# Kernel tuning notes

Measured on AMD Instinct MI355X. Metric: run time of the kernel, lower is better.

Reference implementation:

```python
import jax, jax.numpy as jnp
import numpy as np

ANCHORS = np.array([[4.63,1.97,1.74],[6.93,2.51,2.84],[6.37,2.85,3.19],[10.5,2.94,3.47],
                    [12.29,2.9,3.87],[0.5,2.53,0.98],[2.11,0.77,1.47],[1.7,0.6,1.28],
                    [0.73,0.67,1.77],[0.41,0.41,1.07]], dtype=np.float32)  # [10,3] nuScenes anchor sizes
BINS = 20          # anchor_size_bins
TEXT_DIM = 3 * BINS
NUM_PROPOSALS = 200
NMS_K = 3


def _vector_values():
    la = np.log(ANCHORS)
    return np.linspace(la.min() - 0.1, la.max() - 0.1, BINS).astype(np.float32)


def _anchor_vecs_normed():
    # soft_relu_bin_vectors: soft-bin log-anchors into BINS bins per dim, dim-major flatten
    vals = _vector_values()
    inc = vals[1] - vals[0]
    la = np.log(ANCHORS)                                      # [10,3]
    v = np.clip((la[:, :, None] - vals[None, None, :]) / inc, 0.0, 1.0)  # [10,3,BINS]
    v = v.reshape(10, TEXT_DIM)
    return (v / (1e-8 + np.linalg.norm(v, axis=1, keepdims=True))).astype(np.float32)


def conv2d(x, w, b=None):
    y = jax.lax.conv_general_dilated(x, w, (1, 1), 'SAME',
                                     dimension_numbers=('NCHW', 'OIHW', 'NCHW'))
    if b is not None:
        y = y + b[None, :, None, None]
    return y


def iou_sim_vec(a):
    # vectorized form of the triple-nested loop: prod over dims of min/max ratio
    mn = jnp.minimum(a[:, None, :], a[None, :, :])
    mx = jnp.maximum(a[:, None, :], a[None, :, :])
    return jnp.prod(mn / mx, axis=-1)                         # [10,10]


def setup_inputs() -> dict:
    key = jax.random.key(0)
    ks = jax.random.split(key, 8)
    B, Cin, hid, H, W = 2, 512, 128, 180, 180
    feats = jax.random.normal(ks[0], (B, Cin, H, W), jnp.float32)
    w_shared = jax.random.normal(ks[1], (hid, Cin, 3, 3), jnp.float32) * 0.02
    b_shared = jnp.zeros((hid,), jnp.float32)
    w_bb = jax.random.normal(ks[2], (hid, hid, 3, 3), jnp.float32) * 0.05
    gamma_bb = jnp.ones((hid,), jnp.float32)
    beta_bb = jnp.zeros((hid,), jnp.float32)
    w_hm = jax.random.normal(ks[3], (TEXT_DIM, hid, 3, 3), jnp.float32) * 0.05
    b_hm = jnp.zeros((TEXT_DIM,), jnp.float32)
    thr_scale = jnp.ones((1,), jnp.float32)                   # Threshold2d scale
    logit_scale = jnp.ones((1,), jnp.float32) * np.log(1.0 / 0.07)
    logit_bias = jnp.ones((1,), jnp.float32) * (-10.0)
    w_enc = jax.random.normal(ks[4], (hid, 3), jnp.float32) * 0.1  # Conv1d(3->hid, k=1)
    anchor_vecs = jnp.asarray(_anchor_vecs_normed())
    xs = jnp.arange(W, dtype=jnp.float32) + 0.5
    ys = jnp.arange(H, dtype=jnp.float32) + 0.5
    gy, gx = jnp.meshgrid(ys, xs, indexing='ij')
    bev_pos = jnp.stack([gx.reshape(-1), gy.reshape(-1)], axis=-1)  # [H*W, 2]
    return dict(feats=feats, w_shared=w_shared, b_shared=b_shared, w_bb=w_bb,
                gamma_bb=gamma_bb, beta_bb=beta_bb, w_hm=w_hm, b_hm=b_hm,
                thr_scale=thr_scale, logit_scale=logit_scale, logit_bias=logit_bias,
                w_enc=w_enc, anchor_vecs=anchor_vecs, bev_pos=bev_pos)


def reference(feats, w_shared, b_shared, w_bb, gamma_bb, beta_bb, w_hm, b_hm,
              thr_scale, logit_scale, logit_bias, w_enc, anchor_vecs, bev_pos):
    B, _, H, W = feats.shape
    # shared conv
    lidar_feat = conv2d(feats, w_shared, b_shared)            # [B,hid,H,W]
    # BasicBlock2D: conv + (inference) BN + ReLU
    x = conv2d(lidar_feat, w_bb)
    x = jax.nn.relu(x * gamma_bb[None, :, None, None] + beta_bb[None, :, None, None])
    # heatmap conv -> Threshold2d (sigmoid((x - thresholds) * scale))
    vec = conv2d(x, w_hm, b_hm)                               # [B,60,H,W]
    thresholds = jnp.asarray(np.tile(_vector_values(), 3))[None, :, None, None]
    vec = jax.nn.sigmoid((vec - thresholds) * thr_scale[0])
    # cosine sim vs normalized anchor bin-vectors -> per-class heatmap
    vecn = vec / (1e-8 + jnp.linalg.norm(vec, axis=1, keepdims=True))
    sim = jnp.einsum('bchw,kc->bkhw', vecn, anchor_vecs)      # [B,10,H,W]
    heatmap = jax.nn.sigmoid(logit_scale[0] * sim + logit_bias[0])
    # NMS: keep only local maxima within nms_kernel_size window
    local_max = jax.lax.reduce_window(heatmap, -jnp.inf, jax.lax.max,
                                      (1, 1, NMS_K, NMS_K), (1, 1, 1, 1), 'SAME')
    hm_nms = jnp.where(heatmap == local_max, heatmap, 0.0)
    # top-k proposals over classes x positions
    flat = hm_nms.reshape(B, -1)                              # [B, 10*H*W]
    top_scores, top_idx = jax.lax.top_k(flat, NUM_PROPOSALS)
    top_labels = top_idx // (H * W)                           # [B,P]
    top_pos = top_idx % (H * W)                               # [B,P]
    # gather proposal features, heatmap scores and bev positions
    hid = lidar_feat.shape[1]
    lidar_flat = lidar_feat.reshape(B, hid, H * W)
    idx_f = jnp.broadcast_to(top_pos[:, None, :], (B, hid, NUM_PROPOSALS))
    query_feat = jnp.take_along_axis(lidar_flat, idx_f, axis=2)  # [B,hid,P]
    hm_flat = heatmap.reshape(B, 10, H * W)
    idx_h = jnp.broadcast_to(top_pos[:, None, :], (B, 10, NUM_PROPOSALS))
    query_hm_score = jnp.take_along_axis(hm_flat, idx_h, axis=2)  # [B,10,P]
    query_pos = bev_pos[top_pos]                              # [B,P,2]
    # anchor value encoding (Conv1d(3->hid,k=1) on log-anchor sizes of top classes)
    top_anchor = jnp.log(jnp.asarray(ANCHORS))[top_labels]    # [B,P,3]
    query_feat = query_feat + jnp.einsum('cd,bpd->bcp', w_enc, top_anchor)
    sims = iou_sim_vec(jnp.asarray(ANCHORS))                  # [10,10] anchor IoU similarity
    return heatmap, top_scores, top_labels, query_feat, query_pos, query_hm_score, sims
```

## Files before the change

### kernel.cpp

```cpp
#include <hip/hip_runtime.h>
#include <math.h>


#define HW 180
#define NPIX 32400
#define NCLS 10
#define NPROP 200
#define HID 128
#define TDIM 60
#define NBIG (NCLS*NPIX)

#define TH_LO  (-0.9915981193)
#define TH_STEP (0.1789675812)

__constant__ float c_anchors[10][3] = {
  {4.63f,1.97f,1.74f},{6.93f,2.51f,2.84f},{6.37f,2.85f,3.19f},{10.5f,2.94f,3.47f},
  {12.29f,2.9f,3.87f},{0.5f,2.53f,0.98f},{2.11f,0.77f,1.47f},{1.7f,0.6f,1.28f},
  {0.73f,0.67f,1.77f},{0.41f,0.41f,1.07f}};

using f16x8 = _Float16 __attribute__((ext_vector_type(8)));
using f16x4 = _Float16 __attribute__((ext_vector_type(4)));
using f32x4 = float    __attribute__((ext_vector_type(4)));

#define GLD_LDS16(g, l) __builtin_amdgcn_global_load_lds( \
    (__attribute__((address_space(1))) void*)(g), \
    (__attribute__((address_space(3))) void*)(l), 16, 0, 0)

template<int CIN, int KS, int HALVES>
__global__ void transpose_w_mfma(const float* __restrict__ w, _Float16* __restrict__ dst,
                                 int cout) {
  const int N = HALVES * KS * 36864;
  int i = blockIdx.x * 256 + threadIdx.x;
  if (i >= N) return;
  int j = i & 7;
  int lane = (i >> 3) & 63;
  int mf = (i >> 9) & 3;
  int rest = i >> 11;
  int t = rest % 9; rest /= 9;
  int plane = rest & 1; rest >>= 1;
  int ks = rest % KS; int h = rest / KS;
  int co = h * 64 + mf * 16 + (lane & 15);
  int ch = ks * 32 + (lane >> 4) * 8 + j;
  float v = (co < cout) ? w[((size_t)co * CIN + ch) * 9 + t] : 0.f;
  _Float16 hi = (_Float16)v;
  dst[i] = plane ? (_Float16)(v - (float)hi) : hi;
}

__global__ __launch_bounds__(256)
void convert_feats(const float* __restrict__ feats, _Float16* __restrict__ X1) {
  int px = blockIdx.x * 256 + threadIdx.x;
  int b = blockIdx.y >> 4, ks = blockIdx.y & 15;
  if (px >= NPIX) return;
  const float* src = feats + ((size_t)(b * 512 + ks * 32)) * NPIX + px;
  float v[32];
#pragma unroll
  for (int c = 0; c < 32; ++c) v[c] = src[(size_t)c * NPIX];
  f16x8 hv[4], lv[4];
#pragma unroll
  for (int c = 0; c < 32; ++c) {
    _Float16 h = (_Float16)v[c];
    hv[c >> 3][c & 7] = h;
    lv[c >> 3][c & 7] = (_Float16)(v[c] - (float)h);
  }
  size_t ob = ((size_t)(b * 16 + ks) * NPIX + px) * 32;
#pragma unroll
  for (int i = 0; i < 4; ++i) {
    *(f16x8*)(X1 + ob + i * 8) = hv[i];
    *(f16x8*)(X1 + 33177600u + ob + i * 8) = lv[i];
  }
}

template<int KS, int EPI>
__global__ __launch_bounds__(256, 2)
void conv_mfma(const _Float16* __restrict__ X, const _Float16* __restrict__ W,
               const float* __restrict__ p0, const float* __restrict__ p1,
               float* __restrict__ out0, _Float16* __restrict__ outX,
               const float* __restrict__ thr_scale, const float* __restrict__ logit_scale,
               const float* __restrict__ logit_bias, const float* __restrict__ anchor_vecs) {
  constexpr unsigned XPS = 2u * KS * NPIX * 32;
  extern __shared__ _Float16 dlds[];
  _Float16* lds_x = dlds;
  _Float16* lds_w = dlds + 20736;
  float* lds_av = (float*)(dlds + 39168);

  const int x0 = blockIdx.x * 16;
  const int y0 = blockIdx.y * 16;
  const int b  = (EPI == 2) ? blockIdx.z : (blockIdx.z >> 1);
  const int h  = (EPI == 2) ? 0 : (blockIdx.z & 1);
  const int tid = threadIdx.x;
  const int wave = tid >> 6;
  const int lane = tid & 63;
  const int xl = lane & 15, kg = lane >> 4;

  {
    unsigned* p = (unsigned*)lds_x;
    for (int i = tid; i < 10368; i += 256) p[i] = 0u;
    if (EPI == 2)
      for (int i = tid; i < 600; i += 256) lds_av[i] = anchor_vecs[i];
  }

  unsigned offs[11]; unsigned okb = 0;
#pragma unroll
  for (int s = 0; s < 11; ++s) {
    int inst = wave + 4 * s;
    int c = inst * 64 + lane;
    bool valid = (inst < 41) && (c < 2592);
    int plane = (c >= 1296) ? 1 : 0;
    int cc = c - plane * 1296;
    int px = cc >> 2, q = cc & 3;
    int r = px / 18, xx = px - r * 18;
    int gy = y0 - 1 + r, gx = x0 - 1 + xx;
    bool ok = valid && ((unsigned)gy < 180u) && ((unsigned)gx < 180u);
    offs[s] = ok ? ((unsigned)((b * KS) * NPIX + gy * 180 + gx) * 32u + (unsigned)q * 8u
                    + (unsigned)plane * XPS) : 0u;
    okb |= (ok ? 1u : 0u) << s;
  }

  f32x4 acc[4][4];
#pragma unroll
  for (int mf = 0; mf < 4; ++mf)
#pragma unroll
    for (int f = 0; f < 4; ++f) acc[mf][f] = (f32x4){0.f, 0.f, 0.f, 0.f};

  const _Float16* gwb = W + (size_t)(h * KS) * 36864;
  for (int ks = 0; ks < KS; ++ks) {
    __syncthreads();
    const unsigned kof = (unsigned)ks * (NPIX * 32u);
#pragma unroll
    for (int s = 0; s < 11; ++s) {
      if (okb & (1u << s))
        GLD_LDS16(X + (size_t)(offs[s] + kof), lds_x + (wave + 4 * s) * 512);
    }
    const _Float16* gw = gwb + (size_t)ks * 36864;
#pragma unroll
    for (int s = 0; s < 9; ++s) {
      int c2 = wave + 4 * s;
      GLD_LDS16(gw + c2 * 512 + lane * 8, lds_w + c2 * 512);
    }
    __syncthreads();

#pragma unroll
    for (int t = 0; t < 9; ++t) {
      const int ky = t / 3, kx = t % 3;
      f16x8 bh[4], bl[4];
#pragma unroll
      for (int f = 0; f < 4; ++f) {
        int R = 4 * wave + f;
        int lo = ((R + ky) * 18 + xl + kx) * 32 + kg * 8;
        bh[f] = *(const f16x8*)(lds_x + lo);
        bl[f] = *(const f16x8*)(lds_x + 10368 + lo);
      }
      const _Float16* wt = lds_w + t * 2048 + lane * 8;
      f16x8 ah[4];
#pragma unroll
      for (int mf = 0; mf < 4; ++mf) ah[mf] = *(const f16x8*)(wt + mf * 512);
#pragma unroll
      for (int mf = 0; mf < 4; ++mf)
#pragma unroll
        for (int f = 0; f < 4; ++f) {
          acc[mf][f] = __builtin_amdgcn_mfma_f32_16x16x32_f16(ah[mf], bh[f], acc[mf][f], 0, 0, 0);
          acc[mf][f] = __builtin_amdgcn_mfma_f32_16x16x32_f16(ah[mf], bl[f], acc[mf][f], 0, 0, 0);
        }
    }
    __syncthreads();
#pragma unroll
    for (int s = 0; s < 9; ++s) {
      int c2 = wave + 4 * s;
      GLD_LDS16(gw + 18432 + c2 * 512 + lane * 8, lds_w + c2 * 512);
    }
    __syncthreads();

#pragma unroll
    for (int t = 0; t < 9; ++t) {
      const int ky = t / 3, kx = t % 3;
      f16x8 bh[4];
#pragma unroll
      for (int f = 0; f < 4; ++f) {
        int R = 4 * wave + f;
        int lo = ((R + ky) * 18 + xl + kx) * 32 + kg * 8;
        bh[f] = *(const f16x8*)(lds_x + lo);
      }
      const _Float16* wt = lds_w + t * 2048 + lane * 8;
      f16x8 al[4];
#pragma unroll
      for (int mf = 0; mf < 4; ++mf) al[mf] = *(const f16x8*)(wt + mf * 512);
#pragma unroll
      for (int mf = 0; mf < 4; ++mf)
#pragma unroll
        for (int f = 0; f < 4; ++f)
          acc[mf][f] = __builtin_amdgcn_mfma_f32_16x16x32_f16(al[mf], bh[f], acc[mf][f], 0, 0, 0);
    }
  }

  const int x = x0 + xl;
  if (EPI != 2) {
    if (x >= HW) return;
#pragma unroll
    for (int mf = 0; mf < 4; ++mf) {
      const int cobase = h * 64 + mf * 16 + kg * 4;
      f32x4 q0 = *(const f32x4*)(p0 + cobase);
      f32x4 q1 = (EPI == 1) ? *(const f32x4*)(p1 + cobase) : (f32x4){0.f,0.f,0.f,0.f};
#pragma unroll
      for (int f = 0; f < 4; ++f) {
        const int y = y0 + 4 * wave + f;
        if (y >= HW) continue;
        const int kso = cobase >> 5, c32 = cobase & 31;
        size_t nidx = ((size_t)(b * 4 + kso) * NPIX + (size_t)y * 180 + x) * 32 + c32;
        if (EPI == 0) {
          f32x4 v;
          f16x4 h4, l4;
#pragma unroll
          for (int r = 0; r < 4; ++r) {
            float z = acc[mf][f][r] + q0[r];
            v[r] = z;
            _Float16 hh = (_Float16)z;
            h4[r] = hh;
            l4[r] = (_Float16)(z - (float)hh);
          }
          *(f32x4*)(out0 + nidx) = v;
          *(f16x4*)(outX + nidx) = h4;
          *(f16x4*)(outX + 8294400u + nidx) = l4;
        } else {
          f16x4 h4, l4;
#pragma unroll
          for (int r = 0; r < 4; ++r) {
            float z = fmaf(acc[mf][f][r], q0[r], q1[r]);
            z = fmaxf(z, 0.f);
            _Float16 hh = (_Float16)z;
            h4[r] = hh;
            l4[r] = (_Float16)(z - (float)hh);
          }
          *(f16x4*)(outX + nidx) = h4;
          *(f16x4*)(outX + 8294400u + nidx) = l4;
        }
      }
    }
  } else {
    const float s  = thr_scale[0];
    const float ls = logit_scale[0];
    const float lb = logit_bias[0];
    float bh4[4][4], th4[4][4];
    bool vmask[4];
#pragma unroll
    for (int mf = 0; mf < 4; ++mf) {
      const int cb = mf * 16 + kg * 4;
      vmask[mf] = (cb < TDIM);
#pragma unroll
      for (int r = 0; r < 4; ++r) {
        bh4[mf][r] = vmask[mf] ? p0[cb + r] : 0.f;
        th4[mf][r] = (float)(TH_LO + (double)((cb + r) % 20) * TH_STEP);
      }
    }
#pragma unroll
    for (int f = 0; f < 4; ++f) {
      const int y = y0 + 4 * wave + f;
      float v[4][4];
      float s2 = 0.f;
#pragma unroll
      for (int mf = 0; mf < 4; ++mf)
#pragma unroll
        for (int r = 0; r < 4; ++r) {
          float z = acc[mf][f][r] + bh4[mf][r];
          float t = (z - th4[mf][r]) * s;
          float vv = vmask[mf] ? 1.f / (1.f + expf(-t)) : 0.f;
          v[mf][r] = vv;
          s2 = fmaf(vv, vv, s2);
        }
      s2 += __shfl_xor(s2, 16);
      s2 += __shfl_xor(s2, 32);
      const float rs = 1.f / (1e-8f + sqrtf(s2));
      float hm[10];
#pragma unroll
      for (int k = 0; k < 10; ++k) {
        float d = 0.f;
#pragma unroll
        for (int mf = 0; mf < 4; ++mf) {
          if (true) {
            const int cb = mf * 16 + kg * 4;
            f32x4 a = vmask[mf] ? *(const f32x4*)(lds_av + k * TDIM + cb)
                                : (f32x4){0.f, 0.f, 0.f, 0.f};
#pragma unroll
            for (int r = 0; r < 4; ++r) d = fmaf(v[mf][r], a[r], d);
          }
        }
        d += __shfl_xor(d, 16);
        d += __shfl_xor(d, 32);
        hm[k] = 1.f / (1.f + expf(-fmaf(ls, d * rs, lb)));
      }
      if (y < HW && x < HW) {
#pragma unroll
        for (int j = 0; j < 3; ++j) {
          int k = kg + 4 * j;
          if (k < NCLS)
            out0[((size_t)(b * NCLS + k) * HW + y) * HW + x] = hm[k];
        }
      }
    }
  }
}

__global__ void sims_kernel(float* __restrict__ out_sims) {
  int t = threadIdx.x;
  if (t < 100) {
    int i = t / 10, j = t % 10;
    float r = 1.f;
#pragma unroll
    for (int d = 0; d < 3; ++d) {
      float ai = c_anchors[i][d], aj = c_anchors[j][d];
      r *= fminf(ai, aj) / fmaxf(ai, aj);
    }
    out_sims[t] = r;
  }
}

__global__ __launch_bounds__(256)
void nms_kernel(const float* __restrict__ hm, float* __restrict__ ckey,
                int* __restrict__ cidx, int* __restrict__ cnt) {
  __shared__ int lcnt[2];
  __shared__ int lbase[2];
  const int tid = threadIdx.x;
  if (tid < 2) lcnt[tid] = 0;
  __syncthreads();

  int i = blockIdx.x * 256 + tid;
  bool surv = false; float v = 0.f; int bk = 0, p = 0;
  if (i < 2 * NBIG) {
    int x = i % HW; int y = (i / HW) % HW; int plane = i / NPIX;
    v = hm[i];
    float m = v;
#pragma unroll
    for (int dy = -1; dy <= 1; ++dy)
#pragma unroll
      for (int dx = -1; dx <= 1; ++dx) {
        int yy = y + dy, xx = x + dx;
        if ((unsigned)yy < (unsigned)HW && (unsigned)xx < (unsigned)HW)
          m = fmaxf(m, hm[((size_t)plane * NPIX) + yy * HW + xx]);
      }
    if (v == m) {
      surv = true;
      bk = i / NBIG;
      p = atomicAdd(&lcnt[bk], 1);
    }
  }
  __syncthreads();
  if (tid < 2 && lcnt[tid] > 0)
    lbase[tid] = atomicAdd(&cnt[tid], lcnt[tid]);
  __syncthreads();
  if (surv) {
    int slot = lbase[bk] + p;
    ckey[(size_t)bk * NBIG + slot] = v;
    cidx[(size_t)bk * NBIG + slot] = i - bk * NBIG;
  }
}

__global__ __launch_bounds__(1024)
void topk_kernel(const float* __restrict__ ckey, const int* __restrict__ cidx,
                 const int* __restrict__ cnt, const float* __restrict__ heatmap,
                 const float* __restrict__ bev_pos, float* __restrict__ out,
                 int* __restrict__ iws) {
  const int b = blockIdx.x;
  const int tid = threadIdx.x;
  const float* keys = ckey + (size_t)b * NBIG;
  const int* idxs = cidx + (size_t)b * NBIG;

  __shared__ unsigned hist[256];
  __shared__ unsigned sh_prefix;
  __shared__ int sh_want, sh_n;
  __shared__ int cntGT, cntTie;
  __shared__ unsigned gt_key[256], gt_idx[256];
  __shared__ unsigned tie_idx[2048];

  if (tid == 0) sh_n = cnt[b];
  __syncthreads();
  const int n = sh_n;

  unsigned prefix = 0; int want = NPROP;
  for (int shift = 24; shift >= 0; shift -= 8) {
    if (tid < 256) hist[tid] = 0u;
    __syncthreads();
    for (int i = tid; i < n; i += 1024) {
      unsigned k = __float_as_uint(keys[i]);
      bool match = (shift == 24) || ((k >> (shift + 8)) == (prefix >> (shift + 8)));
      if (match) atomicAdd(&hist[(k >> shift) & 255], 1u);
    }
    __syncthreads();
    if (tid == 0) {
      int cum = 0; int bsel = 0; sh_want = want;
      for (int bin = 255; bin >= 0; --bin) {
        cum += (int)hist[bin];
        if (cum >= want) { bsel = bin; sh_want = want - (cum - (int)hist[bin]); break; }
      }
      sh_prefix = prefix | ((unsigned)bsel << shift);
      cntGT = 0; cntTie = 0;
    }
    __syncthreads();
    prefix = sh_prefix; want = sh_want;
    __syncthreads();
  }
  const unsigned T = prefix;

  for (int i = tid; i < n; i += 1024) {
    unsigned k = __float_as_uint(keys[i]);
    if (k > T) {
      int p = atomicAdd(&cntGT, 1);
      if (p < 256) { gt_key[p] = k; gt_idx[p] = (unsigned)idxs[i]; }
    } else if (k == T) {
      int p = atomicAdd(&cntTie, 1);
      if (p < 2048) tie_idx[p] = (unsigned)idxs[i];
    }
  }
  __syncthreads();
  const int nGT = min(cntGT, 256);
  const int nTie = min(cntTie, 2048);

  for (int i = tid; i < 256; i += 1024)
    if (i >= nGT) { gt_key[i] = 0u; gt_idx[i] = 0xFFFFFFFFu; }
  for (int i = tid; i < 2048; i += 1024)
    if (i >= nTie) tie_idx[i] = 0xFFFFFFFFu;
  __syncthreads();

  for (int k2 = 2; k2 <= 256; k2 <<= 1) {
    for (int j = k2 >> 1; j > 0; j >>= 1) {
      for (int i = tid; i < 256; i += 1024) {
        int ixj = i ^ j;
        if (ixj > i) {
          unsigned ka = gt_key[i], kb = gt_key[ixj];
          unsigned ia = gt_idx[i], ib = gt_idx[ixj];
          bool firstA = (ka > kb) || (ka == kb && ia < ib);
          bool up = ((i & k2) == 0);
          if (up ? !firstA : firstA) {
            gt_key[i] = kb; gt_key[ixj] = ka;
            gt_idx[i] = ib; gt_idx[ixj] = ia;
          }
        }
      }
      __syncthreads();
    }
  }
  for (int k2 = 2; k2 <= 2048; k2 <<= 1) {
    for (int j = k2 >> 1; j > 0; j >>= 1) {
      for (int i = tid; i < 2048; i += 1024) {
        int ixj = i ^ j;
        if (ixj > i) {
          unsigned ia = tie_idx[i], ib = tie_idx[ixj];
          bool firstA = ia < ib;
          bool up = ((i & k2) == 0);
          if (up ? !firstA : firstA) { tie_idx[i] = ib; tie_idx[ixj] = ia; }
        }
      }
      __syncthreads();
    }
  }

  for (int r = tid; r < NPROP; r += 1024) {
    unsigned idx; float score;
    if (r < nGT) { idx = gt_idx[r]; score = __uint_as_float(gt_key[r]); }
    else         { idx = tie_idx[r - nGT]; score = __uint_as_float(T); }
    int label = (int)(idx / NPIX);
    int pos = (int)(idx - (unsigned)label * NPIX);
    out[648000 + b * NPROP + r] = score;
    out[648400 + b * NPROP + r] = (float)label;
    out[700000 + (b * NPROP + r) * 2 + 0] = bev_pos[pos * 2 + 0];
    out[700000 + (b * NPROP + r) * 2 + 1] = bev_pos[pos * 2 + 1];
#pragma unroll
    for (int k = 0; k < NCLS; ++k)
      out[700800 + (b * NCLS + k) * NPROP + r] = heatmap[(size_t)(b * NCLS + k) * NPIX + pos];
    iws[b * NPROP + r] = pos;
    iws[2 * NPROP + b * NPROP + r] = label;
  }
}

__global__ void gather_qf_kernel(const float* __restrict__ lidar, const float* __restrict__ w_enc,
                                 const int* __restrict__ iws, float* __restrict__ out_qf) {
  int p = blockIdx.x % NPROP;
  int b = blockIdx.x / NPROP;
  int c = threadIdx.x;
  int pos = iws[b * NPROP + p];
  int label = iws[2 * NPROP + b * NPROP + p];
  float la0 = logf(c_anchors[label][0]);
  float la1 = logf(c_anchors[label][1]);
  float la2 = logf(c_anchors[label][2]);
  float dot = w_enc[c * 3 + 0] * la0 + w_enc[c * 3 + 1] * la1 + w_enc[c * 3 + 2] * la2;
  float g = lidar[((size_t)(b * 4 + (c >> 5)) * NPIX + pos) * 32 + (c & 31)];
  out_qf[((size_t)b * HID + c) * NPROP + p] = g + dot;
}

extern "C" void kernel_launch(void* const* d_in, const int* in_sizes, int n_in,
                              void* d_out, int out_size, void* d_ws, size_t ws_size,
                              hipStream_t stream) {
  (void)in_sizes; (void)n_in; (void)out_size; (void)ws_size;
  const float* feats       = (const float*)d_in[0];
  const float* w_shared    = (const float*)d_in[1];
  const float* b_shared    = (const float*)d_in[2];
  const float* w_bb        = (const float*)d_in[3];
  const float* gamma_bb    = (const float*)d_in[4];
  const float* beta_bb     = (const float*)d_in[5];
  const float* w_hm        = (const float*)d_in[6];
  const float* b_hm        = (const float*)d_in[7];
  const float* thr_scale   = (const float*)d_in[8];
  const float* logit_scale = (const float*)d_in[9];
  const float* logit_bias  = (const float*)d_in[10];
  const float* w_enc       = (const float*)d_in[11];
  const float* anchor_vecs = (const float*)d_in[12];
  const float* bev_pos     = (const float*)d_in[13];
  float* out = (float*)d_out;

  float* ws = (float*)d_ws;
  size_t off = 0;
  _Float16* X1 = (_Float16*)(ws + off); off += 33177600;
  _Float16* X2 = (_Float16*)(ws + off); off += 8294400;
  float* lidarN = ws + off; off += 8294400;
  _Float16* X3 = (_Float16*)(ws + off); off += 8294400;
  _Float16* W1 = (_Float16*)(ws + off); off += 589824;
  _Float16* W2 = (_Float16*)(ws + off); off += 147456;
  _Float16* W3 = (_Float16*)(ws + off); off += 73728;
  float* ckey  = ws + off; off += (size_t)2 * NBIG;
  int*   cidx  = (int*)(ws + off); off += (size_t)2 * NBIG;
  int*   iws   = (int*)(ws + off); off += 800;
  int*   cnt   = (int*)(ws + off);

  transpose_w_mfma<512,16,2><<<(2*16*36864 + 255)/256, 256, 0, stream>>>(w_shared, W1, 128);
  transpose_w_mfma<128, 4,2><<<(2*4*36864  + 255)/256, 256, 0, stream>>>(w_bb, W2, 128);
  transpose_w_mfma<128, 4,1><<<(1*4*36864  + 255)/256, 256, 0, stream>>>(w_hm, W3, 60);
  convert_feats<<<dim3(127, 32), 256, 0, stream>>>(feats, X1);

  const unsigned CONV_LDS = (20736 + 18432) * sizeof(_Float16);
  const unsigned HEAD_LDS = CONV_LDS + 600 * sizeof(float);
  dim3 cgrid(12, 12, 4);
  conv_mfma<16,0><<<cgrid, 256, CONV_LDS, stream>>>(X1, W1, b_shared, nullptr, lidarN, X2,
                                                    nullptr, nullptr, nullptr, nullptr);
  conv_mfma<4, 1><<<cgrid, 256, CONV_LDS, stream>>>(X2, W2, gamma_bb, beta_bb, nullptr, X3,
                                                    nullptr, nullptr, nullptr, nullptr);
  dim3 hgrid(12, 12, 2);
  conv_mfma<4, 2><<<hgrid, 256, HEAD_LDS, stream>>>(X3, W3, b_hm, nullptr, out, nullptr,
                                                    thr_scale, logit_scale, logit_bias,
                                                    anchor_vecs);

  sims_kernel<<<1, 128, 0, stream>>>(out + 704800);
  hipMemsetAsync(cnt, 0, 2 * sizeof(int), stream);
  nms_kernel<<<(2*NBIG + 255)/256, 256, 0, stream>>>(out, ckey, cidx, cnt);
  topk_kernel<<<2, 1024, 0, stream>>>(ckey, cidx, cnt, out, bev_pos, out, iws);
  gather_qf_kernel<<<2*NPROP, 128, 0, stream>>>(lidarN, w_enc, iws, out + 648800);
}
```

Before: 586.3 us.

## Restructure conv MFMA loop by kernel column to reuse input fragments across rows

Permutes the weight layout so taps are grouped by kernel column (kx), then splits each channel slice into three phases of 3 taps. Each phase loads hi and lo weight planes together, and the six input row fragments are read from LDS once and reused across the three ky taps. The hi and lo weight passes are also merged into one loop. This cuts redundant LDS reads of input fragments and the LDS weight footprint, in exchange for more barriers per K-slice (3 syncs instead of 2 weight loads) and more live registers.

```diff
diff --git a/kernel.cpp b/kernel.cpp
--- a/kernel.cpp
+++ b/kernel.cpp
@@ -36,7 +36,8 @@
   int lane = (i >> 3) & 63;
   int mf = (i >> 9) & 3;
   int rest = i >> 11;
-  int t = rest % 9; rest /= 9;
+  int tsl = rest % 9; rest /= 9;
+  int t = (tsl % 3) * 3 + (tsl / 3);
   int plane = rest & 1; rest >>= 1;
   int ks = rest % KS; int h = rest / KS;
   int co = h * 64 + mf * 16 + (lane & 15);
@@ -81,7 +82,7 @@
   extern __shared__ _Float16 dlds[];
   _Float16* lds_x = dlds;
   _Float16* lds_w = dlds + 20736;
-  float* lds_av = (float*)(dlds + 39168);
+  float* lds_av = (float*)(dlds + 33024);
 
   const int x0 = blockIdx.x * 16;
   const int y0 = blockIdx.y * 16;
@@ -124,71 +125,52 @@
 
   const _Float16* gwb = W + (size_t)(h * KS) * 36864;
   for (int ks = 0; ks < KS; ++ks) {
-    __syncthreads();
     const unsigned kof = (unsigned)ks * (NPIX * 32u);
-#pragma unroll
-    for (int s = 0; s < 11; ++s) {
-      if (okb & (1u << s))
-        GLD_LDS16(X + (size_t)(offs[s] + kof), lds_x + (wave + 4 * s) * 512);
-    }
     const _Float16* gw = gwb + (size_t)ks * 36864;
 #pragma unroll
-    for (int s = 0; s < 9; ++s) {
-      int c2 = wave + 4 * s;
-      GLD_LDS16(gw + c2 * 512 + lane * 8, lds_w + c2 * 512);
-    }
-    __syncthreads();
-
-#pragma unroll
-    for (int t = 0; t < 9; ++t) {
-      const int ky = t / 3, kx = t % 3;
-      f16x8 bh[4], bl[4];
-#pragma unroll
-      for (int f = 0; f < 4; ++f) {
-        int R = 4 * wave + f;
-        int lo = ((R + ky) * 18 + xl + kx) * 32 + kg * 8;
-        bh[f] = *(const f16x8*)(lds_x + lo);
-        bl[f] = *(const f16x8*)(lds_x + 10368 + lo);
-      }
-      const _Float16* wt = lds_w + t * 2048 + lane * 8;
-      f16x8 ah[4];
-#pragma unroll
-      for (int mf = 0; mf < 4; ++mf) ah[mf] = *(const f16x8*)(wt + mf * 512);
-#pragma unroll
-      for (int mf = 0; mf < 4; ++mf)
-#pragma unroll
-        for (int f = 0; f < 4; ++f) {
-          acc[mf][f] = __builtin_amdgcn_mfma_f32_16x16x32_f16(ah[mf], bh[f], acc[mf][f], 0, 0, 0);
-          acc[mf][f] = __builtin_amdgcn_mfma_f32_16x16x32_f16(ah[mf], bl[f], acc[mf][f], 0, 0, 0);
-        }
-    }
-    __syncthreads();
-#pragma unroll
-    for (int s = 0; s < 9; ++s) {
-      int c2 = wave + 4 * s;
-      GLD_LDS16(gw + 18432 + c2 * 512 + lane * 8, lds_w + c2 * 512);
-    }
-    __syncthreads();
-
-#pragma unroll
-    for (int t = 0; t < 9; ++t) {
-      const int ky = t / 3, kx = t % 3;
-      f16x8 bh[4];
-#pragma unroll
-      for (int f = 0; f < 4; ++f) {
-        int R = 4 * wave + f;
-        int lo = ((R + ky) * 18 + xl + kx) * 32 + kg * 8;
-        bh[f] = *(const f16x8*)(lds_x + lo);
-      }
-      const _Float16* wt = lds_w + t * 2048 + lane * 8;
-      f16x8 al[4];
-#pragma unroll
-      for (int mf = 0; mf < 4; ++mf) al[mf] = *(const f16x8*)(wt + mf * 512);
-#pragma unroll
-      for (int mf = 0; mf < 4; ++mf)
-#pragma unroll
-        for (int f = 0; f < 4; ++f)
-          acc[mf][f] = __builtin_amdgcn_mfma_f32_16x16x32_f16(al[mf], bh[f], acc[mf][f], 0, 0, 0);
+    for (int g = 0; g < 3; ++g) {
+      __syncthreads();
+      if (g == 0) {
+#pragma unroll
+        for (int s = 0; s < 11; ++s) {
+          if (okb & (1u << s))
+            GLD_LDS16(X + (size_t)(offs[s] + kof), lds_x + (wave + 4 * s) * 512);
+        }
+      }
+#pragma unroll
+      for (int s = 0; s < 6; ++s) {
+        int c2 = wave + 4 * s;
+        int pl = c2 / 12, idx = c2 - pl * 12;
+        GLD_LDS16(gw + pl * 18432 + g * 6144 + idx * 512 + lane * 8,
+                  lds_w + pl * 6144 + idx * 512);
+      }
+      __syncthreads();
+
+      f16x8 bfh[6], bfl[6];
+#pragma unroll
+      for (int rr = 0; rr < 6; ++rr) {
+        int lo = ((4 * wave + rr) * 18 + xl + g) * 32 + kg * 8;
+        bfh[rr] = *(const f16x8*)(lds_x + lo);
+        bfl[rr] = *(const f16x8*)(lds_x + 10368 + lo);
+      }
+#pragma unroll
+      for (int ky = 0; ky < 3; ++ky) {
+        const _Float16* wt = lds_w + ky * 2048 + lane * 8;
+        f16x8 ah[4], al[4];
+#pragma unroll
+        for (int mf = 0; mf < 4; ++mf) {
+          ah[mf] = *(const f16x8*)(wt + mf * 512);
+          al[mf] = *(const f16x8*)(wt + 6144 + mf * 512);
+        }
+#pragma unroll
+        for (int mf = 0; mf < 4; ++mf)
+#pragma unroll
+          for (int f = 0; f < 4; ++f) {
+            acc[mf][f] = __builtin_amdgcn_mfma_f32_16x16x32_f16(ah[mf], bfh[f + ky], acc[mf][f], 0, 0, 0);
+            acc[mf][f] = __builtin_amdgcn_mfma_f32_16x16x32_f16(ah[mf], bfl[f + ky], acc[mf][f], 0, 0, 0);
+            acc[mf][f] = __builtin_amdgcn_mfma_f32_16x16x32_f16(al[mf], bfh[f + ky], acc[mf][f], 0, 0, 0);
+          }
+      }
     }
   }
 
@@ -275,13 +257,11 @@
         float d = 0.f;
 #pragma unroll
         for (int mf = 0; mf < 4; ++mf) {
-          if (true) {
-            const int cb = mf * 16 + kg * 4;
-            f32x4 a = vmask[mf] ? *(const f32x4*)(lds_av + k * TDIM + cb)
-                                : (f32x4){0.f, 0.f, 0.f, 0.f};
-#pragma unroll
-            for (int r = 0; r < 4; ++r) d = fmaf(v[mf][r], a[r], d);
-          }
+          const int cb = mf * 16 + kg * 4;
+          f32x4 a = vmask[mf] ? *(const f32x4*)(lds_av + k * TDIM + cb)
+                              : (f32x4){0.f, 0.f, 0.f, 0.f};
+#pragma unroll
+          for (int r = 0; r < 4; ++r) d = fmaf(v[mf][r], a[r], d);
         }
         d += __shfl_xor(d, 16);
         d += __shfl_xor(d, 32);
@@ -524,7 +504,7 @@
   transpose_w_mfma<128, 4,1><<<(1*4*36864  + 255)/256, 256, 0, stream>>>(w_hm, W3, 60);
   convert_feats<<<dim3(127, 32), 256, 0, stream>>>(feats, X1);
 
-  const unsigned CONV_LDS = (20736 + 18432) * sizeof(_Float16);
+  const unsigned CONV_LDS = (20736 + 12288) * sizeof(_Float16);
   const unsigned HEAD_LDS = CONV_LDS + 600 * sizeof(float);
   dim3 cgrid(12, 12, 4);
   conv_mfma<16,0><<<cgrid, 256, CONV_LDS, stream>>>(X1, W1, b_shared, nullptr, lidarN, X2,
```

Result: no change. 585.9 us (-0.1%).
